# Performance work log

Measured on AMD Instinct MI355X. Metric: run time of the kernel, lower is better.

The kernel has to match this reference:

```python
import jax, jax.numpy as jnp
import numpy as np


def hard_sigmoid(x):
    # clamp(0.2*x + 0.5, 0, 1) -- Theano/lwtnn convention
    return jnp.clip(0.2 * x + 0.5, 0.0, 1.0)


def setup_inputs() -> dict:
    key = jax.random.key(0)
    ks = jax.random.split(key, 10)
    B, T, D, H = 128, 1024, 256, 256
    s_in = 1.0 / np.sqrt(D)
    s_h = 1.0 / np.sqrt(H)
    return {
        "x": jax.random.normal(ks[0], (B, T, D), dtype=jnp.float32),
        "W_z": jax.random.normal(ks[1], (D, H), dtype=jnp.float32) * s_in,
        "W_r": jax.random.normal(ks[2], (D, H), dtype=jnp.float32) * s_in,
        "W_h": jax.random.normal(ks[3], (D, H), dtype=jnp.float32) * s_in,
        "U_z": jax.random.normal(ks[4], (H, H), dtype=jnp.float32) * s_h,
        "U_r": jax.random.normal(ks[5], (H, H), dtype=jnp.float32) * s_h,
        "U_h": jax.random.normal(ks[6], (H, H), dtype=jnp.float32) * s_h,
        "b_z": jax.random.normal(ks[7], (H,), dtype=jnp.float32) * 0.01,
        "b_r": jax.random.normal(ks[8], (H,), dtype=jnp.float32) * 0.01,
        "b_h": jax.random.normal(ks[9], (H,), dtype=jnp.float32) * 0.01,
    }


def reference(x, W_z, W_r, W_h, U_z, U_r, U_h, b_z, b_r, b_h):
    B, T, D = x.shape
    H = W_z.shape[1]
    # Precompute input projections for all timesteps in one big GEMM each
    # (same math as per-step xt @ W_* in the original loop).
    xz = jnp.einsum("btd,dh->bth", x, W_z) + b_z  # [B,T,H]
    xr = jnp.einsum("btd,dh->bth", x, W_r) + b_r
    xh = jnp.einsum("btd,dh->bth", x, W_h) + b_h

    def step(h, inputs):
        xz_t, xr_t, xh_t = inputs  # each [B,H]
        z = hard_sigmoid(xz_t + h @ U_z)
        r = hard_sigmoid(xr_t + h @ U_r)
        hh = jnp.tanh(xh_t + (r * h) @ U_h)
        h_new = z * h + (1.0 - z) * hh
        return h_new, None

    h0 = jnp.zeros((B, H), dtype=x.dtype)
    # scan over time axis: move T to leading axis
    xs = (xz.swapaxes(0, 1), xr.swapaxes(0, 1), xh.swapaxes(0, 1))
    h_final, _ = jax.lax.scan(step, h0, xs)
    return h_final
```

## Files before the change

kernel.cpp:

```cpp
#include <hip/hip_runtime.h>
#include <hip/hip_bf16.h>
#include <math.h>

#define BB 128
#define TT 1024
#define DD 256
#define HH 256
#define MM (BB * TT)
#define NN3 768

typedef __attribute__((ext_vector_type(8))) short short8;
typedef __attribute__((ext_vector_type(4))) float f32x4;
typedef __attribute__((address_space(1))) unsigned int gu32;
typedef __attribute__((address_space(3))) unsigned int lu32;

static __device__ __forceinline__ float bf2f(unsigned int u16) {
    return __uint_as_float(u16 << 16);
}
static __device__ __forceinline__ unsigned short f2bf(float f) {
    unsigned int u = __float_as_uint(f);
    unsigned int r = u + 0x7FFFu + ((u >> 16) & 1u);
    return (unsigned short)(r >> 16);
}
static __device__ __forceinline__ unsigned short f2bf_fast(float f) {
    return (unsigned short)((__float_as_uint(f) + 0x8000u) >> 16);
}

static __device__ __forceinline__ void barrier_lgkm() {
    asm volatile("s_waitcnt lgkmcnt(0)\n\ts_barrier" ::: "memory");
}
static __device__ __forceinline__ void barrier_full() {
    asm volatile("s_waitcnt vmcnt(0) lgkmcnt(0)\n\ts_barrier" ::: "memory");
}

__global__ __launch_bounds__(256) void wb_kernel(
    const float* __restrict__ Wz, const float* __restrict__ Wr,
    const float* __restrict__ Wh, unsigned short* __restrict__ Wb)
{
    int n = blockIdx.x;
    int g = n >> 8, col = n & 255;
    const float* W = (g == 0) ? Wz : (g == 1 ? Wr : Wh);
    int k = threadIdx.x;
    Wb[(size_t)n * 256 + k] = f2bf(W[(size_t)k * HH + col]);
}

__global__ __launch_bounds__(256)
__attribute__((amdgpu_waves_per_eu(2, 2)))
void xproj_mfma(
    const float* __restrict__ x, const unsigned short* __restrict__ Wb,
    const float* __restrict__ bz, const float* __restrict__ br,
    const float* __restrict__ bh, unsigned short* __restrict__ xw)
{
    const int tid  = threadIdx.x;
    const int lane = tid & 63;
    const int wv   = tid >> 6;
    const int nq   = lane & 15;
    const int kq   = lane >> 4;

    const int n0  = blockIdx.x * 64;
    const int m0  = blockIdx.y * 128;
    const int g   = n0 >> 8;
    const int nc0 = n0 & 255;
    const float* bias = (g == 0) ? bz : (g == 1 ? br : bh);

    short8 wf[8][4];
#pragma unroll
    for (int c = 0; c < 8; ++c)
#pragma unroll
        for (int nt = 0; nt < 4; ++nt)
            wf[c][nt] = *(const short8*)&Wb[(size_t)(n0 + nt * 16 + nq) * 256
                                            + c * 32 + kq * 8];
    float bv[4];
#pragma unroll
    for (int nt = 0; nt < 4; ++nt) bv[nt] = bias[nc0 + nt * 16 + nq];

    f32x4 acc[2][4];
#pragma unroll
    for (int mi = 0; mi < 2; ++mi)
#pragma unroll
        for (int nt = 0; nt < 4; ++nt) acc[mi][nt] = (f32x4){0.f, 0.f, 0.f, 0.f};

    const int mrow0 = m0 + wv * 32;

#pragma unroll
    for (int c = 0; c < 8; ++c) {
        short8 af[2];
#pragma unroll
        for (int mi = 0; mi < 2; ++mi) {
            const float* xp = &x[(size_t)(mrow0 + mi * 16 + nq) * 256
                                 + c * 32 + kq * 8];
            float4 f0 = *(const float4*)xp;
            float4 f1 = *(const float4*)(xp + 4);
            short8 a;
            a[0] = (short)f2bf(f0.x); a[1] = (short)f2bf(f0.y);
            a[2] = (short)f2bf(f0.z); a[3] = (short)f2bf(f0.w);
            a[4] = (short)f2bf(f1.x); a[5] = (short)f2bf(f1.y);
            a[6] = (short)f2bf(f1.z); a[7] = (short)f2bf(f1.w);
            af[mi] = a;
        }
#pragma unroll
        for (int mi = 0; mi < 2; ++mi)
#pragma unroll
            for (int nt = 0; nt < 4; ++nt)
                acc[mi][nt] = __builtin_amdgcn_mfma_f32_16x16x32_bf16(
                    af[mi], wf[c][nt], acc[mi][nt], 0, 0, 0);
    }

    const int t0   = (m0 & 1023) + wv * 32;
    const int b    = m0 >> 10;
    const int bid  = b >> 4;
    const int brow = b & 15;
    const int lane4 = (brow >> 2) * 16 + nq;
    const int ii    = brow & 3;

#pragma unroll
    for (int mi = 0; mi < 2; ++mi)
#pragma unroll
        for (int nt = 0; nt < 4; ++nt) {
            int ti = g * 16 + (nc0 >> 4) + nt;
#pragma unroll
            for (int i = 0; i < 4; ++i) {
                int t = t0 + mi * 16 + kq * 4 + i;
                size_t addr = (size_t)(t * 8 + bid) * 12288
                              + (size_t)(ti * 256 + lane4 * 4 + ii);
                xw[addr] = f2bf(acc[mi][nt][i] + bv[nt]);
            }
        }
}

__global__ __launch_bounds__(512)
__attribute__((amdgpu_waves_per_eu(2, 2)))
void gru_rec_kernel(
    const unsigned short* __restrict__ xw,
    const float* __restrict__ Uz, const float* __restrict__ Ur,
    const float* __restrict__ Uh,
    float* __restrict__ out)
{
    __shared__ unsigned short xstage[2][12288];
    __shared__ short hA[16][264];
    __shared__ short rhA[16][264];

    const int tid  = threadIdx.x;
    const int lane = tid & 63;
    const int wv   = tid >> 6;
    const int nq   = lane & 15;
    const int kq   = lane >> 4;
    const int bid  = blockIdx.x;

    short8 wzr[4][8];
#pragma unroll
    for (int q = 0; q < 4; ++q) {
        const float* U = (q < 2) ? Uz : Ur;
        const int col0 = (wv + 8 * (q & 1)) * 16;
#pragma unroll
        for (int c = 0; c < 8; ++c) {
            short8 f;
#pragma unroll
            for (int j = 0; j < 8; ++j)
                f[j] = (short)f2bf(U[(size_t)(c * 32 + kq * 8 + j) * HH + col0 + nq]);
            wzr[q][c] = f;
        }
    }
    short8 wh[2][8];
#pragma unroll
    for (int tj = 0; tj < 2; ++tj) {
        const int col0 = (wv + 8 * tj) * 16;
#pragma unroll
        for (int c = 0; c < 8; ++c) {
            short8 f;
#pragma unroll
            for (int j = 0; j < 8; ++j)
                f[j] = (short)f2bf(Uh[(size_t)(c * 32 + kq * 8 + j) * HH + col0 + nq]);
            wh[tj][c] = f;
        }
    }

    for (int idx = tid; idx < 16 * 264; idx += 512) ((short*)hA)[idx] = 0;
    float hprev[8];
#pragma unroll
    for (int i = 0; i < 8; ++i) hprev[i] = 0.f;

    auto stage = [&](int t, int buf) {
        const char* gsrc = (const char*)(xw + (size_t)(t * 8 + bid) * 12288);
        char* lbase = (char*)&xstage[buf][0];
        int woff = wv * 3072;
#pragma unroll
        for (int ld = 0; ld < 3; ++ld) {
            int off = woff + ld * 1024;
            __builtin_amdgcn_global_load_lds(
                (const gu32*)(gsrc + off + lane * 16),
                (lu32*)(lbase + off), 16, 0, 0);
        }
    };

    stage(0, 0);
    barrier_full();

    const int tiz = wv;
    auto step = [&](int t, int par) {
        int tn2 = (t + 1 < TT) ? (t + 1) : (TT - 1);
        stage(tn2, par ^ 1);

        const unsigned short* xs = &xstage[par][0];

        f32x4 accA[4];
#pragma unroll
        for (int q = 0; q < 4; ++q) {
            int ti = (q < 2 ? 0 : 16) + tiz + 8 * (q & 1);
            uint2 u = *(const uint2*)&xs[(ti * 64 + lane) * 4];
            accA[q][0] = bf2f(u.x & 0xffffu);
            accA[q][1] = bf2f(u.x >> 16);
            accA[q][2] = bf2f(u.y & 0xffffu);
            accA[q][3] = bf2f(u.y >> 16);
        }
#pragma unroll
        for (int c = 0; c < 8; ++c) {
            short8 af = *(const short8*)&hA[nq][c * 32 + kq * 8];
#pragma unroll
            for (int q = 0; q < 4; ++q)
                accA[q] = __builtin_amdgcn_mfma_f32_16x16x32_bf16(
                    af, wzr[q][c], accA[q], 0, 0, 0);
        }

#pragma unroll
        for (int tj = 0; tj < 2; ++tj) {
            int col = (tiz + 8 * tj) * 16 + nq;
#pragma unroll
            for (int i = 0; i < 4; ++i) {
                float r = __builtin_amdgcn_fmed3f(
                    __builtin_fmaf(0.2f, accA[2 + tj][i], 0.5f), 0.f, 1.f);
                rhA[kq * 4 + i][col] = (short)f2bf_fast(r * hprev[tj * 4 + i]);
            }
        }
        barrier_lgkm();

        f32x4 accH[2];
#pragma unroll
        for (int tj = 0; tj < 2; ++tj) {
            int ti = 32 + tiz + 8 * tj;
            uint2 u = *(const uint2*)&xs[(ti * 64 + lane) * 4];
            accH[tj][0] = bf2f(u.x & 0xffffu);
            accH[tj][1] = bf2f(u.x >> 16);
            accH[tj][2] = bf2f(u.y & 0xffffu);
            accH[tj][3] = bf2f(u.y >> 16);
        }
#pragma unroll
        for (int c = 0; c < 8; ++c) {
            short8 af = *(const short8*)&rhA[nq][c * 32 + kq * 8];
            accH[0] = __builtin_amdgcn_mfma_f32_16x16x32_bf16(af, wh[0][c], accH[0], 0, 0, 0);
            accH[1] = __builtin_amdgcn_mfma_f32_16x16x32_bf16(af, wh[1][c], accH[1], 0, 0, 0);
        }

#pragma unroll
        for (int tj = 0; tj < 2; ++tj) {
            int col = (tiz + 8 * tj) * 16 + nq;
#pragma unroll
            for (int i = 0; i < 4; ++i) {
                int idx = tj * 4 + i;
                float z = __builtin_amdgcn_fmed3f(
                    __builtin_fmaf(0.2f, accA[tj][i], 0.5f), 0.f, 1.f);
                float a = __builtin_amdgcn_fmed3f(accH[tj][i], -12.f, 12.f);
                float e  = exp2f(a * 2.88539008f);
                float hh = __builtin_fmaf(-2.f, __builtin_amdgcn_rcpf(e + 1.f), 1.f);
                float hn = __builtin_fmaf(z, hprev[idx] - hh, hh);
                hprev[idx] = hn;
                hA[kq * 4 + i][col] = (short)f2bf_fast(hn);
            }
        }
        barrier_full();
    };

    for (int t = 0; t < TT; t += 2) {
        step(t, 0);
        step(t + 1, 1);
    }

#pragma unroll
    for (int tj = 0; tj < 2; ++tj) {
        int col = (tiz + 8 * tj) * 16 + nq;
#pragma unroll
        for (int i = 0; i < 4; ++i)
            out[(size_t)(bid * 16 + kq * 4 + i) * HH + col] = hprev[tj * 4 + i];
    }
}

extern "C" void kernel_launch(void* const* d_in, const int* in_sizes, int n_in,
                              void* d_out, int out_size, void* d_ws, size_t ws_size,
                              hipStream_t stream) {
    const float* x  = (const float*)d_in[0];
    const float* Wz = (const float*)d_in[1];
    const float* Wr = (const float*)d_in[2];
    const float* Wh = (const float*)d_in[3];
    const float* Uz = (const float*)d_in[4];
    const float* Ur = (const float*)d_in[5];
    const float* Uh = (const float*)d_in[6];
    const float* bz = (const float*)d_in[7];
    const float* br = (const float*)d_in[8];
    const float* bh = (const float*)d_in[9];
    float* out = (float*)d_out;

    unsigned short* xw = (unsigned short*)d_ws;
    unsigned short* Wb =
        (unsigned short*)((char*)d_ws + (size_t)MM * NN3 * sizeof(unsigned short));

    wb_kernel<<<NN3, 256, 0, stream>>>(Wz, Wr, Wh, Wb);

    dim3 g1(NN3 / 64, MM / 128);
    xproj_mfma<<<g1, 256, 0, stream>>>(x, Wb, bz, br, bh, xw);

    gru_rec_kernel<<<8, 512, 0, stream>>>(xw, Uz, Ur, Uh, out);
}
```

Baseline: 2.977 ms.

## Split GRU recurrence across 16 waves, one 16-column tile each

Doubles the recurrent kernel's block to 1024 threads so each of 16 waves owns a single 16-column tile of z, r and h instead of two. This halves the serial MFMA chain and gate math per wave on every timestep, which is the latency-bound critical path. Register-resident weights per wave drop accordingly, and staging is spread over 12 waves. In exchange, barriers now synchronize twice as many waves, and each wave has fewer independent MFMAs to hide latency.

```diff
diff --git a/kernel.cpp b/kernel.cpp
--- a/kernel.cpp
+++ b/kernel.cpp
@@ -128,8 +128,8 @@
         }
 }
 
-__global__ __launch_bounds__(512)
-__attribute__((amdgpu_waves_per_eu(2, 2)))
+__global__ __launch_bounds__(1024)
+__attribute__((amdgpu_waves_per_eu(4, 4)))
 void gru_rec_kernel(
     const unsigned short* __restrict__ xw,
     const float* __restrict__ Uz, const float* __restrict__ Ur,
@@ -146,126 +146,103 @@
     const int nq   = lane & 15;
     const int kq   = lane >> 4;
     const int bid  = blockIdx.x;
-
-    short8 wzr[4][8];
-#pragma unroll
-    for (int q = 0; q < 4; ++q) {
-        const float* U = (q < 2) ? Uz : Ur;
-        const int col0 = (wv + 8 * (q & 1)) * 16;
-#pragma unroll
-        for (int c = 0; c < 8; ++c) {
-            short8 f;
-#pragma unroll
-            for (int j = 0; j < 8; ++j)
-                f[j] = (short)f2bf(U[(size_t)(c * 32 + kq * 8 + j) * HH + col0 + nq]);
-            wzr[q][c] = f;
-        }
+    const int col0 = wv * 16;
+
+    short8 wz[8], wr[8], whv[8];
+#pragma unroll
+    for (int c = 0; c < 8; ++c) {
+        short8 fz, fr, fh;
+#pragma unroll
+        for (int j = 0; j < 8; ++j) {
+            size_t rowoff = (size_t)(c * 32 + kq * 8 + j) * HH + col0 + nq;
+            fz[j] = (short)f2bf(Uz[rowoff]);
+            fr[j] = (short)f2bf(Ur[rowoff]);
+            fh[j] = (short)f2bf(Uh[rowoff]);
+        }
+        wz[c] = fz; wr[c] = fr; whv[c] = fh;
     }
-    short8 wh[2][8];
-#pragma unroll
-    for (int tj = 0; tj < 2; ++tj) {
-        const int col0 = (wv + 8 * tj) * 16;
-#pragma unroll
-        for (int c = 0; c < 8; ++c) {
-            short8 f;
-#pragma unroll
-            for (int j = 0; j < 8; ++j)
-                f[j] = (short)f2bf(Uh[(size_t)(c * 32 + kq * 8 + j) * HH + col0 + nq]);
-            wh[tj][c] = f;
-        }
-    }
-
-    for (int idx = tid; idx < 16 * 264; idx += 512) ((short*)hA)[idx] = 0;
-    float hprev[8];
-#pragma unroll
-    for (int i = 0; i < 8; ++i) hprev[i] = 0.f;
+
+    for (int idx = tid; idx < 16 * 264; idx += 1024) ((short*)hA)[idx] = 0;
+    float hprev[4];
+#pragma unroll
+    for (int i = 0; i < 4; ++i) hprev[i] = 0.f;
 
     auto stage = [&](int t, int buf) {
-        const char* gsrc = (const char*)(xw + (size_t)(t * 8 + bid) * 12288);
-        char* lbase = (char*)&xstage[buf][0];
-        int woff = wv * 3072;
-#pragma unroll
-        for (int ld = 0; ld < 3; ++ld) {
-            int off = woff + ld * 1024;
-            __builtin_amdgcn_global_load_lds(
-                (const gu32*)(gsrc + off + lane * 16),
-                (lu32*)(lbase + off), 16, 0, 0);
+        if (wv < 12) {
+            const char* gsrc = (const char*)(xw + (size_t)(t * 8 + bid) * 12288);
+            char* lbase = (char*)&xstage[buf][0];
+            int woff = wv * 2048;
+#pragma unroll
+            for (int ld = 0; ld < 2; ++ld) {
+                int off = woff + ld * 1024;
+                __builtin_amdgcn_global_load_lds(
+                    (const gu32*)(gsrc + off + lane * 16),
+                    (lu32*)(lbase + off), 16, 0, 0);
+            }
         }
     };
 
     stage(0, 0);
     barrier_full();
 
-    const int tiz = wv;
     auto step = [&](int t, int par) {
         int tn2 = (t + 1 < TT) ? (t + 1) : (TT - 1);
         stage(tn2, par ^ 1);
 
         const unsigned short* xs = &xstage[par][0];
 
-        f32x4 accA[4];
-#pragma unroll
-        for (int q = 0; q < 4; ++q) {
-            int ti = (q < 2 ? 0 : 16) + tiz + 8 * (q & 1);
-            uint2 u = *(const uint2*)&xs[(ti * 64 + lane) * 4];
-            accA[q][0] = bf2f(u.x & 0xffffu);
-            accA[q][1] = bf2f(u.x >> 16);
-            accA[q][2] = bf2f(u.y & 0xffffu);
-            accA[q][3] = bf2f(u.y >> 16);
+        f32x4 accZ, accR;
+        {
+            uint2 uz = *(const uint2*)&xs[((0  + wv) * 64 + lane) * 4];
+            uint2 ur = *(const uint2*)&xs[((16 + wv) * 64 + lane) * 4];
+            accZ[0] = bf2f(uz.x & 0xffffu);
+            accZ[1] = bf2f(uz.x >> 16);
+            accZ[2] = bf2f(uz.y & 0xffffu);
+            accZ[3] = bf2f(uz.y >> 16);
+            accR[0] = bf2f(ur.x & 0xffffu);
+            accR[1] = bf2f(ur.x >> 16);
+            accR[2] = bf2f(ur.y & 0xffffu);
+            accR[3] = bf2f(ur.y >> 16);
         }
 #pragma unroll
         for (int c = 0; c < 8; ++c) {
             short8 af = *(const short8*)&hA[nq][c * 32 + kq * 8];
-#pragma unroll
-            for (int q = 0; q < 4; ++q)
-                accA[q] = __builtin_amdgcn_mfma_f32_16x16x32_bf16(
-                    af, wzr[q][c], accA[q], 0, 0, 0);
-        }
-
-#pragma unroll
-        for (int tj = 0; tj < 2; ++tj) {
-            int col = (tiz + 8 * tj) * 16 + nq;
-#pragma unroll
-            for (int i = 0; i < 4; ++i) {
-                float r = __builtin_amdgcn_fmed3f(
-                    __builtin_fmaf(0.2f, accA[2 + tj][i], 0.5f), 0.f, 1.f);
-                rhA[kq * 4 + i][col] = (short)f2bf_fast(r * hprev[tj * 4 + i]);
-            }
+            accZ = __builtin_amdgcn_mfma_f32_16x16x32_bf16(af, wz[c], accZ, 0, 0, 0);
+            accR = __builtin_amdgcn_mfma_f32_16x16x32_bf16(af, wr[c], accR, 0, 0, 0);
+        }
+
+#pragma unroll
+        for (int i = 0; i < 4; ++i) {
+            float r = __builtin_amdgcn_fmed3f(
+                __builtin_fmaf(0.2f, accR[i], 0.5f), 0.f, 1.f);
+            rhA[kq * 4 + i][col0 + nq] = (short)f2bf_fast(r * hprev[i]);
         }
         barrier_lgkm();
 
-        f32x4 accH[2];
-#pragma unroll
-        for (int tj = 0; tj < 2; ++tj) {
-            int ti = 32 + tiz + 8 * tj;
-            uint2 u = *(const uint2*)&xs[(ti * 64 + lane) * 4];
-            accH[tj][0] = bf2f(u.x & 0xffffu);
-            accH[tj][1] = bf2f(u.x >> 16);
-            accH[tj][2] = bf2f(u.y & 0xffffu);
-            accH[tj][3] = bf2f(u.y >> 16);
+        f32x4 accH;
+        {
+            uint2 u = *(const uint2*)&xs[((32 + wv) * 64 + lane) * 4];
+            accH[0] = bf2f(u.x & 0xffffu);
+            accH[1] = bf2f(u.x >> 16);
+            accH[2] = bf2f(u.y & 0xffffu);
+            accH[3] = bf2f(u.y >> 16);
         }
 #pragma unroll
         for (int c = 0; c < 8; ++c) {
             short8 af = *(const short8*)&rhA[nq][c * 32 + kq * 8];
-            accH[0] = __builtin_amdgcn_mfma_f32_16x16x32_bf16(af, wh[0][c], accH[0], 0, 0, 0);
-            accH[1] = __builtin_amdgcn_mfma_f32_16x16x32_bf16(af, wh[1][c], accH[1], 0, 0, 0);
-        }
-
-#pragma unroll
-        for (int tj = 0; tj < 2; ++tj) {
-            int col = (tiz + 8 * tj) * 16 + nq;
-#pragma unroll
-            for (int i = 0; i < 4; ++i) {
-                int idx = tj * 4 + i;
-                float z = __builtin_amdgcn_fmed3f(
-                    __builtin_fmaf(0.2f, accA[tj][i], 0.5f), 0.f, 1.f);
-                float a = __builtin_amdgcn_fmed3f(accH[tj][i], -12.f, 12.f);
-                float e  = exp2f(a * 2.88539008f);
-                float hh = __builtin_fmaf(-2.f, __builtin_amdgcn_rcpf(e + 1.f), 1.f);
-                float hn = __builtin_fmaf(z, hprev[idx] - hh, hh);
-                hprev[idx] = hn;
-                hA[kq * 4 + i][col] = (short)f2bf_fast(hn);
-            }
+            accH = __builtin_amdgcn_mfma_f32_16x16x32_bf16(af, whv[c], accH, 0, 0, 0);
+        }
+
+#pragma unroll
+        for (int i = 0; i < 4; ++i) {
+            float z = __builtin_amdgcn_fmed3f(
+                __builtin_fmaf(0.2f, accZ[i], 0.5f), 0.f, 1.f);
+            float a = __builtin_amdgcn_fmed3f(accH[i], -12.f, 12.f);
+            float e  = exp2f(a * 2.88539008f);
+            float hh = __builtin_fmaf(-2.f, __builtin_amdgcn_rcpf(e + 1.f), 1.f);
+            float hn = __builtin_fmaf(z, hprev[i] - hh, hh);
+            hprev[i] = hn;
+            hA[kq * 4 + i][col0 + nq] = (short)f2bf_fast(hn);
         }
         barrier_full();
     };
@@ -276,12 +253,8 @@
     }
 
 #pragma unroll
-    for (int tj = 0; tj < 2; ++tj) {
-        int col = (tiz + 8 * tj) * 16 + nq;
-#pragma unroll
-        for (int i = 0; i < 4; ++i)
-            out[(size_t)(bid * 16 + kq * 4 + i) * HH + col] = hprev[tj * 4 + i];
-    }
+    for (int i = 0; i < 4; ++i)
+        out[(size_t)(bid * 16 + kq * 4 + i) * HH + col0 + nq] = hprev[i];
 }
 
 extern "C" void kernel_launch(void* const* d_in, const int* in_sizes, int n_in,
@@ -308,5 +281,5 @@
     dim3 g1(NN3 / 64, MM / 128);
     xproj_mfma<<<g1, 256, 0, stream>>>(x, Wb, bz, br, bh, xw);
 
-    gru_rec_kernel<<<8, 512, 0, stream>>>(xw, Uz, Ur, Uh, out);
-}
+    gru_rec_kernel<<<8, 1024, 0, stream>>>(xw, Uz, Ur, Uh, out);
+}
```

After: 2.828 ms. 1.05x faster.
